# Performance work log

Measured on AMD Instinct MI355X. Metric: run time of the kernel, lower is better.

Reference implementation:

```python
import jax, jax.numpy as jnp
import numpy as np

FG_THRESH = 0.5
BG_THRESH = 0.4
REG_W = (10.0, 10.0, 5.0, 5.0)
SMOOTH_L1_BETA = 1.0 / 9.0


def box_iou(a, b):
    # a: [G,4], b: [T,4] -> [G,T]
    area_a = (a[:, 2] - a[:, 0]) * (a[:, 3] - a[:, 1])
    area_b = (b[:, 2] - b[:, 0]) * (b[:, 3] - b[:, 1])
    lt = jnp.maximum(a[:, None, :2], b[None, :, :2])
    rb = jnp.minimum(a[:, None, 2:], b[None, :, 2:])
    wh = jnp.clip(rb - lt, 0.0)
    inter = wh[..., 0] * wh[..., 1]
    return inter / (area_a[:, None] + area_b[None, :] - inter)


def elementwise_iou(a, b):
    # a, b: [T,4] -> [T]
    area_a = (a[:, 2] - a[:, 0]) * (a[:, 3] - a[:, 1])
    area_b = (b[:, 2] - b[:, 0]) * (b[:, 3] - b[:, 1])
    lt = jnp.maximum(a[:, :2], b[:, :2])
    rb = jnp.minimum(a[:, 2:], b[:, 2:])
    wh = jnp.clip(rb - lt, 0.0)
    inter = wh[:, 0] * wh[:, 1]
    return inter / (area_a + area_b - inter)


def encode_boxes(ref_boxes, proposals):
    # torchvision BoxCoder.encode with weights (10,10,5,5)
    wx, wy, ww, wh = REG_W
    ex_w = proposals[:, 2] - proposals[:, 0]
    ex_h = proposals[:, 3] - proposals[:, 1]
    ex_cx = proposals[:, 0] + 0.5 * ex_w
    ex_cy = proposals[:, 1] + 0.5 * ex_h
    gt_w = ref_boxes[:, 2] - ref_boxes[:, 0]
    gt_h = ref_boxes[:, 3] - ref_boxes[:, 1]
    gt_cx = ref_boxes[:, 0] + 0.5 * gt_w
    gt_cy = ref_boxes[:, 1] + 0.5 * gt_h
    dx = wx * (gt_cx - ex_cx) / ex_w
    dy = wy * (gt_cy - ex_cy) / ex_h
    dw = ww * jnp.log(gt_w / ex_w)
    dh = wh * jnp.log(gt_h / ex_h)
    return jnp.stack([dx, dy, dw, dh], axis=1)


def _match_and_targets(all_props, gtb, gtl):
    # all_props: [T,4], gtb: [G,4], gtl: [G]
    iou = box_iou(gtb, all_props)                       # [G,T]
    matched_vals = jnp.max(iou, axis=0)                 # [T]
    matched_idxs = jnp.argmax(iou, axis=0)              # [T] (clamped match)
    labels = gtl[matched_idxs].astype(jnp.int32)
    labels = jnp.where(matched_vals < BG_THRESH, 0, labels)          # background
    labels = jnp.where((matched_vals >= BG_THRESH) & (matched_vals < FG_THRESH), -1, labels)  # ignore
    matched_gt = gtb[matched_idxs]                      # [T,4]
    reg_targets = encode_boxes(matched_gt, all_props)   # [T,4]
    score_targets = elementwise_iou(matched_gt, all_props)  # [T]
    return labels, reg_targets, score_targets


def _losses(proposals, gt_boxes, gt_labels, class_logits, box_regression, box_scores):
    B = proposals.shape[0]
    # add_gt_proposals: concat gt boxes onto proposals
    all_props = jnp.concatenate([proposals, gt_boxes], axis=1)  # [B,T,4]
    labels, reg_t, bs_t = jax.vmap(_match_and_targets)(all_props, gt_boxes, gt_labels)

    C = class_logits.shape[-1]
    N = B * class_logits.shape[1]
    labels = labels.reshape(-1)                         # [N]
    logits = class_logits.reshape(N, C)
    breg = box_regression.reshape(N, C, 4)
    bsc = box_scores.reshape(-1)
    reg_t = reg_t.reshape(N, 4)
    bs_t = bs_t.reshape(-1)

    valid = labels >= 0
    pos = labels > 0
    n_valid = jnp.maximum(jnp.sum(valid), 1).astype(logits.dtype)
    n_pos = jnp.maximum(jnp.sum(pos), 1).astype(logits.dtype)
    safe_lab = jnp.clip(labels, 0, C - 1)

    # classification: cross-entropy over non-ignored rois
    logp = jax.nn.log_softmax(logits, axis=-1)
    nll = -jnp.take_along_axis(logp, safe_lab[:, None], axis=1)[:, 0]
    cls_loss = jnp.sum(jnp.where(valid, nll, 0.0)) / n_valid

    pred_reg = jnp.take_along_axis(breg, safe_lab[:, None, None], axis=1)[:, 0]  # [N,4]
    diff = jnp.abs(pred_reg - reg_t)
    sl1 = jnp.where(diff < SMOOTH_L1_BETA, 0.5 * diff * diff / SMOOTH_L1_BETA, diff - 0.5 * SMOOTH_L1_BETA)
    box_loss = jnp.sum(jnp.where(pos[:, None], sl1, 0.0)) / n_valid

    # box score: L1 between predicted score and IoU target on positives
    score_loss = jnp.sum(jnp.where(pos, jnp.abs(bsc - bs_t), 0.0)) / n_pos

    return jnp.stack([cls_loss, box_loss, score_loss])


def setup_inputs() -> dict:
    key = jax.random.key(0)
    ks = jax.random.split(key, 6)
    B, P, G, C = 8, 8000, 100, 81

    def make_boxes(k, shape):
        k1, k2, k3, k4 = jax.random.split(k, 4)
        x1 = jax.random.uniform(k1, shape) * 800.0
        y1 = jax.random.uniform(k2, shape) * 600.0
        w = 8.0 + jax.random.uniform(k3, shape) * 192.0
        h = 8.0 + jax.random.uniform(k4, shape) * 192.0
        return jnp.stack([x1, y1, x1 + w, y1 + h], axis=-1)

    return {
        "proposals": make_boxes(ks[0], (B, P)),
        "gt_boxes": make_boxes(ks[1], (B, G)),
        "gt_labels": jax.random.randint(ks[2], (B, G), 1, C),
        "class_logits": jax.random.normal(ks[3], (B, P + G, C), dtype=jnp.float32),
        "box_regression": jax.random.normal(ks[4], (B, P + G, C * 4), dtype=jnp.float32) * 0.1,
        "box_scores": jax.random.uniform(ks[5], (B, P + G)),
    }


def reference(proposals, gt_boxes, gt_labels, class_logits, box_regression, box_scores):
    return _losses(proposals, gt_boxes, gt_labels, class_logits, box_regression, box_scores)
```

## Files before the change

kernel.cpp:

```cpp
#include <hip/hip_runtime.h>
#include <math.h>

namespace {
constexpr int kB = 8;
constexpr int kP = 8000;
constexpr int kG = 100;
constexpr int kT = kP + kG;
constexpr int kC = 81;
constexpr int kBlk = 256;
constexpr int kLanes = 16;
constexpr int kGroups = kBlk / kLanes;
constexpr int kBlocksPerBatch = 256;
constexpr int kNBlk = kB * kBlocksPerBatch;
constexpr int kStride = 2048;
constexpr float kFG = 0.5f;
constexpr float kBG = 0.4f;
constexpr float kBeta = 1.0f / 9.0f;
}

template <int C>
__device__ __forceinline__ float dppf(float v) {
  return __int_as_float(
      __builtin_amdgcn_update_dpp(0, __float_as_int(v), C, 0xF, 0xF, true));
}
template <int C>
__device__ __forceinline__ int dppi(int v) {
  return __builtin_amdgcn_update_dpp(0, v, C, 0xF, 0xF, true);
}
#define ROR8 0x128
#define ROR4 0x124
#define ROR2 0x122
#define ROR1 0x121

__global__ __launch_bounds__(kBlk, 6) void roi_partials(
    const float* __restrict__ proposals,
    const float* __restrict__ gt_boxes,
    const int*   __restrict__ gt_labels,
    const float* __restrict__ class_logits,
    const float* __restrict__ box_reg,
    const float* __restrict__ box_scores,
    float* __restrict__ partials)
{
  __shared__ float4 s_gt[kG];
  __shared__ float  s_area[kG];
  __shared__ int    s_lab[kG];
  __shared__ float  s_red[kBlk / 64][5];

  const int l      = threadIdx.x & (kLanes - 1);
  const int grp    = threadIdx.x >> 4;
  const int b      = blockIdx.x >> 8;
  const int blk_in = blockIdx.x & (kBlocksPerBatch - 1);
  const int t0     = blk_in * (2 * kGroups) + grp;
  const int t1     = t0 + kGroups;
  const bool in0   = t0 < kT;
  const bool in1   = t1 < kT;
  const int r0     = b * kT + t0;
  const int r1     = b * kT + t1;

  float4 pb0 = make_float4(0.f, 0.f, 0.f, 0.f);
  float4 pb1 = make_float4(0.f, 0.f, 0.f, 0.f);
  if (in0 && t0 < kP)
    pb0 = reinterpret_cast<const float4*>(proposals)[(size_t)b * kP + t0];
  if (in1 && t1 < kP)
    pb1 = reinterpret_cast<const float4*>(proposals)[(size_t)b * kP + t1];
  float x0[6], x1[6], bs0 = 0.f, bs1 = 0.f;
  #pragma unroll
  for (int k = 0; k < 6; ++k) { x0[k] = -INFINITY; x1[k] = -INFINITY; }
  if (in0) {
    const float* lg = class_logits + (size_t)r0 * kC;
    #pragma unroll
    for (int k = 0; k < 5; ++k) x0[k] = lg[l + k * kLanes];
    if (l == 0) x0[5] = lg[80];
    bs0 = box_scores[r0];
  }
  if (in1) {
    const float* lg = class_logits + (size_t)r1 * kC;
    #pragma unroll
    for (int k = 0; k < 5; ++k) x1[k] = lg[l + k * kLanes];
    if (l == 0) x1[5] = lg[80];
    bs1 = box_scores[r1];
  }

  for (int i = threadIdx.x; i < kG; i += kBlk) {
    const float4 g = reinterpret_cast<const float4*>(gt_boxes)[(size_t)b * kG + i];
    s_gt[i] = g;
    s_area[i] = (g.z - g.x) * (g.w - g.y);
    s_lab[i] = gt_labels[b * kG + i];
  }
  __syncthreads();
  if (in0 && t0 >= kP) pb0 = s_gt[t0 - kP];
  if (in1 && t1 >= kP) pb1 = s_gt[t1 - kP];

  float a_nll = 0.f, a_sl1 = 0.f, a_sc = 0.f, a_cv = 0.f, a_cp = 0.f;

  auto do_tile = [&](bool in, int r, const float4& pb, const float* x,
                     float bs) {
    if (!in) return;
    const float area_p = (pb.z - pb.x) * (pb.w - pb.y);

    float best = -1.f;
    int bi = 0;
    #pragma unroll
    for (int k = 0; k < 7; ++k) {
      const int g = l + k * kLanes;
      if (k < 6 || g < kG) {
        const float4 gb = s_gt[g];
        float w = fminf(gb.z, pb.z) - fmaxf(gb.x, pb.x);
        float h = fminf(gb.w, pb.w) - fmaxf(gb.y, pb.y);
        w = fmaxf(w, 0.f);
        h = fmaxf(h, 0.f);
        const float inter = w * h;
        const float iou =
            inter * __builtin_amdgcn_rcpf(s_area[g] + area_p - inter);
        if (iou > best) { best = iou; bi = g; }
      }
    }
    #define ARGMAX_STEP(C)                                                 \
      {                                                                    \
        const float ob = dppf<C>(best);                                    \
        const int   oi = dppi<C>(bi);                                      \
        if (ob > best || (ob == best && oi < bi)) { best = ob; bi = oi; }  \
      }
    ARGMAX_STEP(ROR8)
    ARGMAX_STEP(ROR4)
    ARGMAX_STEP(ROR2)
    ARGMAX_STEP(ROR1)
    #undef ARGMAX_STEP

    int label = s_lab[bi];
    if (best < kBG) label = 0;
    else if (best < kFG) label = -1;
    const bool valid = label >= 0;
    const bool pos = label > 0;
    const int lab = valid ? label : 0;

    float se = 0.f;
    #pragma unroll
    for (int k = 0; k < 6; ++k) se += __expf(x[k]);
    se += dppf<ROR8>(se);
    se += dppf<ROR4>(se);
    se += dppf<ROR2>(se);
    se += dppf<ROR1>(se);
    if (valid && l == 0) {
      const float xl = class_logits[(size_t)r * kC + lab];
      a_nll += __logf(se) - xl;
      a_cv += 1.f;
    }

    if (pos && l == 0) {
      const float4 gb = s_gt[bi];
      const float ex_w = pb.z - pb.x, ex_h = pb.w - pb.y;
      const float ex_cx = pb.x + 0.5f * ex_w, ex_cy = pb.y + 0.5f * ex_h;
      const float gt_w = gb.z - gb.x, gt_h = gb.w - gb.y;
      const float gt_cx = gb.x + 0.5f * gt_w, gt_cy = gb.y + 0.5f * gt_h;
      const float tx = 10.f * (gt_cx - ex_cx) / ex_w;
      const float ty = 10.f * (gt_cy - ex_cy) / ex_h;
      const float tw = 5.f * __logf(gt_w / ex_w);
      const float th = 5.f * __logf(gt_h / ex_h);
      const float4 pv =
          reinterpret_cast<const float4*>(box_reg)[(size_t)r * kC + lab];
      const float d0 = fabsf(pv.x - tx), d1 = fabsf(pv.y - ty);
      const float d2 = fabsf(pv.z - tw), d3 = fabsf(pv.w - th);
      float acc = 0.f;
      acc += (d0 < kBeta) ? 4.5f * d0 * d0 : d0 - 0.5f * kBeta;
      acc += (d1 < kBeta) ? 4.5f * d1 * d1 : d1 - 0.5f * kBeta;
      acc += (d2 < kBeta) ? 4.5f * d2 * d2 : d2 - 0.5f * kBeta;
      acc += (d3 < kBeta) ? 4.5f * d3 * d3 : d3 - 0.5f * kBeta;
      a_sl1 += acc;
      a_sc += fabsf(bs - best);
      a_cp += 1.f;
    }
  };

  do_tile(in0, r0, pb0, x0, bs0);
  do_tile(in1, r1, pb1, x1, bs1);

  float vals[5] = {a_nll, a_sl1, a_sc, a_cv, a_cp};
  #pragma unroll
  for (int j = 0; j < 5; ++j) {
    vals[j] += __shfl_down(vals[j], 32, 64);
    vals[j] += __shfl_down(vals[j], 16, 64);
  }
  const int wave = threadIdx.x >> 6, lane = threadIdx.x & 63;
  if (lane == 0) {
    #pragma unroll
    for (int j = 0; j < 5; ++j) s_red[wave][j] = vals[j];
  }
  __syncthreads();
  if (threadIdx.x == 0) {
    #pragma unroll
    for (int j = 0; j < 5; ++j) {
      const float tot = s_red[0][j] + s_red[1][j] + s_red[2][j] + s_red[3][j];
      partials[j * kStride + blockIdx.x] = tot;
    }
  }
}

__global__ __launch_bounds__(1024) void roi_finalize(
    const float* __restrict__ partials, float* __restrict__ out) {
  __shared__ float s_red[16][5];
  float vals[5];
  #pragma unroll
  for (int j = 0; j < 5; ++j)
    vals[j] = partials[j * kStride + threadIdx.x] +
              partials[j * kStride + threadIdx.x + 1024];
  #pragma unroll
  for (int off = 32; off > 0; off >>= 1) {
    #pragma unroll
    for (int j = 0; j < 5; ++j) vals[j] += __shfl_down(vals[j], off, 64);
  }
  const int wave = threadIdx.x >> 6, lane = threadIdx.x & 63;
  if (lane == 0) {
    #pragma unroll
    for (int j = 0; j < 5; ++j) s_red[wave][j] = vals[j];
  }
  __syncthreads();
  if (threadIdx.x == 0) {
    float tot[5];
    #pragma unroll
    for (int j = 0; j < 5; ++j) {
      float s = 0.f;
      #pragma unroll
      for (int w = 0; w < 16; ++w) s += s_red[w][j];
      tot[j] = s;
    }
    const float nv = fmaxf(tot[3], 1.f);
    const float np = fmaxf(tot[4], 1.f);
    out[0] = tot[0] / nv;
    out[1] = tot[1] / nv;
    out[2] = tot[2] / np;
  }
}

extern "C" void kernel_launch(void* const* d_in, const int* in_sizes, int n_in,
                              void* d_out, int out_size, void* d_ws, size_t ws_size,
                              hipStream_t stream) {
  (void)in_sizes; (void)n_in; (void)out_size; (void)ws_size;
  const float* proposals    = (const float*)d_in[0];
  const float* gt_boxes     = (const float*)d_in[1];
  const int*   gt_labels    = (const int*)d_in[2];
  const float* class_logits = (const float*)d_in[3];
  const float* box_reg      = (const float*)d_in[4];
  const float* box_scores   = (const float*)d_in[5];
  float* partials = (float*)d_ws;
  float* out = (float*)d_out;

  roi_partials<<<kNBlk, kBlk, 0, stream>>>(proposals, gt_boxes, gt_labels,
                                           class_logits, box_reg, box_scores,
                                           partials);
  roi_finalize<<<1, 1024, 0, stream>>>(partials, out);
}
```

Measured before the change: 19.65 us.

## Fuse finalize into main kernel via atomic slots and last-block reduction

The separate finalize kernel is removed. Each block atomically adds its five partial sums into 32 striped slots, bumps a global counter, and the last block to arrive reads the slots and writes the final losses. This is meant to remove the second kernel launch and its dependency gap. In exchange it adds a memset on the stream, contended float atomics, and float summation whose order now depends on block arrival, so the result is no longer deterministic.

```diff
diff --git a/kernel.cpp b/kernel.cpp
--- a/kernel.cpp
+++ b/kernel.cpp
@@ -12,7 +12,7 @@
 constexpr int kGroups = kBlk / kLanes;
 constexpr int kBlocksPerBatch = 256;
 constexpr int kNBlk = kB * kBlocksPerBatch;
-constexpr int kStride = 2048;
+constexpr int kSlots = 32;
 constexpr float kFG = 0.5f;
 constexpr float kBG = 0.4f;
 constexpr float kBeta = 1.0f / 9.0f;
@@ -32,19 +32,23 @@
 #define ROR2 0x122
 #define ROR1 0x121
 
-__global__ __launch_bounds__(kBlk, 6) void roi_partials(
+__global__ __launch_bounds__(kBlk, 6) void roi_fused(
     const float* __restrict__ proposals,
     const float* __restrict__ gt_boxes,
     const int*   __restrict__ gt_labels,
     const float* __restrict__ class_logits,
     const float* __restrict__ box_reg,
     const float* __restrict__ box_scores,
-    float* __restrict__ partials)
+    float* __restrict__ acc,
+    unsigned int* __restrict__ counter,
+    float* __restrict__ out)
 {
   __shared__ float4 s_gt[kG];
   __shared__ float  s_area[kG];
   __shared__ int    s_lab[kG];
   __shared__ float  s_red[kBlk / 64][5];
+  __shared__ float  s_fin[5 * kSlots];
+  __shared__ bool   s_last;
 
   const int l      = threadIdx.x & (kLanes - 1);
   const int grp    = threadIdx.x >> 4;
@@ -161,12 +165,12 @@
           reinterpret_cast<const float4*>(box_reg)[(size_t)r * kC + lab];
       const float d0 = fabsf(pv.x - tx), d1 = fabsf(pv.y - ty);
       const float d2 = fabsf(pv.z - tw), d3 = fabsf(pv.w - th);
-      float acc = 0.f;
-      acc += (d0 < kBeta) ? 4.5f * d0 * d0 : d0 - 0.5f * kBeta;
-      acc += (d1 < kBeta) ? 4.5f * d1 * d1 : d1 - 0.5f * kBeta;
-      acc += (d2 < kBeta) ? 4.5f * d2 * d2 : d2 - 0.5f * kBeta;
-      acc += (d3 < kBeta) ? 4.5f * d3 * d3 : d3 - 0.5f * kBeta;
-      a_sl1 += acc;
+      float s = 0.f;
+      s += (d0 < kBeta) ? 4.5f * d0 * d0 : d0 - 0.5f * kBeta;
+      s += (d1 < kBeta) ? 4.5f * d1 * d1 : d1 - 0.5f * kBeta;
+      s += (d2 < kBeta) ? 4.5f * d2 * d2 : d2 - 0.5f * kBeta;
+      s += (d3 < kBeta) ? 4.5f * d3 * d3 : d3 - 0.5f * kBeta;
+      a_sl1 += s;
       a_sc += fabsf(bs - best);
       a_cp += 1.f;
     }
@@ -187,48 +191,39 @@
     for (int j = 0; j < 5; ++j) s_red[wave][j] = vals[j];
   }
   __syncthreads();
+
   if (threadIdx.x == 0) {
+    const int slot = blockIdx.x & (kSlots - 1);
     #pragma unroll
     for (int j = 0; j < 5; ++j) {
       const float tot = s_red[0][j] + s_red[1][j] + s_red[2][j] + s_red[3][j];
-      partials[j * kStride + blockIdx.x] = tot;
-    }
-  }
-}
-
-__global__ __launch_bounds__(1024) void roi_finalize(
-    const float* __restrict__ partials, float* __restrict__ out) {
-  __shared__ float s_red[16][5];
-  float vals[5];
-  #pragma unroll
-  for (int j = 0; j < 5; ++j)
-    vals[j] = partials[j * kStride + threadIdx.x] +
-              partials[j * kStride + threadIdx.x + 1024];
-  #pragma unroll
-  for (int off = 32; off > 0; off >>= 1) {
-    #pragma unroll
-    for (int j = 0; j < 5; ++j) vals[j] += __shfl_down(vals[j], off, 64);
-  }
-  const int wave = threadIdx.x >> 6, lane = threadIdx.x & 63;
-  if (lane == 0) {
-    #pragma unroll
-    for (int j = 0; j < 5; ++j) s_red[wave][j] = vals[j];
+      atomicAdd(&acc[j * kSlots + slot], tot);
+    }
+    asm volatile("s_waitcnt vmcnt(0)" ::: "memory");
+    const unsigned int old = __hip_atomic_fetch_add(
+        counter, 1u, __ATOMIC_RELAXED, __HIP_MEMORY_SCOPE_AGENT);
+    s_last = (old == (unsigned int)(kNBlk - 1));
   }
   __syncthreads();
-  if (threadIdx.x == 0) {
-    float tot[5];
-    #pragma unroll
-    for (int j = 0; j < 5; ++j) {
-      float s = 0.f;
+
+  if (s_last) {
+    if (threadIdx.x < 5 * kSlots)
+      s_fin[threadIdx.x] = atomicAdd(&acc[threadIdx.x], 0.0f);
+    __syncthreads();
+    if (threadIdx.x == 0) {
+      float tot[5];
       #pragma unroll
-      for (int w = 0; w < 16; ++w) s += s_red[w][j];
-      tot[j] = s;
-    }
-    const float nv = fmaxf(tot[3], 1.f);
-    const float np = fmaxf(tot[4], 1.f);
-    out[0] = tot[0] / nv;
-    out[1] = tot[1] / nv;
-    out[2] = tot[2] / np;
+      for (int j = 0; j < 5; ++j) {
+        float s = 0.f;
+        for (int k = 0; k < kSlots; ++k) s += s_fin[j * kSlots + k];
+        tot[j] = s;
+      }
+      const float nv = fmaxf(tot[3], 1.f);
+      const float np = fmaxf(tot[4], 1.f);
+      out[0] = tot[0] / nv;
+      out[1] = tot[1] / nv;
+      out[2] = tot[2] / np;
+    }
   }
 }
 
@@ -242,11 +237,13 @@
   const float* class_logits = (const float*)d_in[3];
   const float* box_reg      = (const float*)d_in[4];
   const float* box_scores   = (const float*)d_in[5];
-  float* partials = (float*)d_ws;
+
+  float* acc = (float*)d_ws;
+  unsigned int* counter = (unsigned int*)((char*)d_ws + 1024);
   float* out = (float*)d_out;
 
-  roi_partials<<<kNBlk, kBlk, 0, stream>>>(proposals, gt_boxes, gt_labels,
-                                           class_logits, box_reg, box_scores,
-                                           partials);
-  roi_finalize<<<1, 1024, 0, stream>>>(partials, out);
-}
+  hipMemsetAsync(d_ws, 0, 1024 + sizeof(unsigned int), stream);
+  roi_fused<<<kNBlk, kBlk, 0, stream>>>(proposals, gt_boxes, gt_labels,
+                                        class_logits, box_reg, box_scores,
+                                        acc, counter, out);
+}
```

Result: slower. 42.37 us (+115.6%).
